# Optimization experiments

Hardware: AMD Instinct MI355X
Metric: run time of the kernel (lower is better)

## Reference

```python
import jax, jax.numpy as jnp
import numpy as np

B, T, NC, WD, UNITS = 128, 256, 128, 512, 512
IN_DIM = NC + WD + NC  # x_char + x_word + one-hot prev word


def setup_inputs() -> dict:
    key = jax.random.key(0)
    ks = jax.random.split(key, 7)
    scale = 0.05  # keep gates out of saturation
    return {
        "x_char": jax.random.normal(ks[0], (B, T, NC), jnp.float32),
        "x_word": jax.random.normal(ks[1], (B, T, WD), jnp.float32),
        "W": jax.random.normal(ks[2], (IN_DIM, 4 * UNITS), jnp.float32) * scale,
        "U": jax.random.normal(ks[3], (UNITS, 4 * UNITS), jnp.float32) * scale,
        "b": jnp.zeros((4 * UNITS,), jnp.float32),
        "Ws": jax.random.normal(ks[4], (UNITS, NC), jnp.float32) * scale,
        "bs": jnp.zeros((NC,), jnp.float32),
    }


def reference(x_char, x_word, W, U, b, Ws, bs):
    Bsz, Tlen, nclasses = x_char.shape
    units = U.shape[0]
    # time-major, concat char+word features (matches x_shuffled in original)
    x_t = jnp.concatenate(
        [jnp.swapaxes(x_char, 0, 1), jnp.swapaxes(x_word, 0, 1)], axis=-1
    )  # [T, B, NC+WD]
    word0 = jnp.full((Bsz, nclasses), 1e-5, x_char.dtype)  # start_char
    h0 = jnp.zeros((Bsz, units), x_char.dtype)
    c0 = jnp.zeros((Bsz, units), x_char.dtype)

    def step(carry, x_i):
        word_vec, h, c = carry
        ins = jnp.concatenate([x_i, word_vec], axis=1)  # [B, IN_DIM]
        z = ins @ W + h @ U + b  # [B, 4*units]; Keras gate order i,f,c,o
        zi, zf, zg, zo = jnp.split(z, 4, axis=1)
        i = jax.nn.sigmoid(zi)
        f = jax.nn.sigmoid(zf)
        g = jnp.tanh(zg)
        o = jax.nn.sigmoid(zo)
        c_new = f * c + i * g
        h_new = o * jnp.tanh(c_new)
        probs = jax.nn.softmax(h_new @ Ws + bs, axis=-1)
        idx = jnp.argmax(probs, axis=1)  # [B]
        word_vec_new = jax.nn.one_hot(idx, nclasses, dtype=x_char.dtype)
        return (word_vec_new, h_new, c_new), idx

    _, idxs = jax.lax.scan(step, (word0, h0, c0), x_t)  # idxs: [T, B]
    return jnp.swapaxes(idxs, 0, 1)  # [B, T] int word indices
```

## Files before the change

### kernel.cpp

```cpp
#include <hip/hip_runtime.h>
#include <math.h>

#define BSZ   128
#define TLEN  256
#define NCLS  128
#define WDIM  512
#define XDIM  640
#define G4    2048

#define BT    16
#define JTS   16
#define NBLK  256
#define NTHR  512
#define KCH   8

#define H_OFF    0
#define LOG_OFF  131072
#define W0_OFF   180224
#define FLAG_OFF 182272

typedef unsigned long long ull;

__device__ __forceinline__ float sigmoidf_(float x) {
  return 1.0f / (1.0f + expf(-x));
}

__device__ __forceinline__ float4 ld_dev16(const float* p) {
  const ull* q = (const ull*)p;
  ull a = __hip_atomic_load(q,     __ATOMIC_RELAXED, __HIP_MEMORY_SCOPE_AGENT);
  ull b = __hip_atomic_load(q + 1, __ATOMIC_RELAXED, __HIP_MEMORY_SCOPE_AGENT);
  float4 r;
  ((ull*)&r)[0] = a;
  ((ull*)&r)[1] = b;
  return r;
}

__global__ void setup_kernel(const float* __restrict__ W,
                             const float* __restrict__ bias,
                             float* __restrict__ ws) {
  int tid = blockIdx.x * blockDim.x + threadIdx.x;
  for (int i = tid; i < 3 * BSZ * NCLS; i += 64 * 256)
    ws[LOG_OFF + i] = 0.0f;
  if (tid < 4096)
    ((unsigned int*)(ws + FLAG_OFF))[tid] = 0u;
  if (tid < G4) {
    float s = 0.0f;
    #pragma unroll 4
    for (int r = 0; r < NCLS; ++r)
      s += W[(size_t)(XDIM + r) * G4 + tid];
    ws[W0_OFF + tid] = bias[tid] + 1e-5f * s;
  }
}

__global__ void __launch_bounds__(NTHR, 1)
lstm_main(const float* __restrict__ xc, const float* __restrict__ xw,
          const float* __restrict__ W,  const float* __restrict__ U,
          const float* __restrict__ bias, const float* __restrict__ Wsm,
          const float* __restrict__ bsv, int* __restrict__ out,
          float* __restrict__ ws)
{
  __shared__ float U_lds[512 * 64];
  __shared__ float ins_lds[2][2176];
  __shared__ float wsm_lds[16 * 128];
  __shared__ float hl_lds[16 * 17];
  __shared__ int   idx_lds[BT];

  float* zred  = &ins_lds[0][0];
  float* Wt    = &ins_lds[0][0];
  float* red_v = zred;
  int*   red_i = (int*)(zred + 528);

  const int tid = threadIdx.x;
  const int blk = blockIdx.x;
  const int grp = blk & 7;
  const int jt  = blk >> 3;
  const int b0  = grp * BT;
  const int j0  = jt * JTS;

  const int gb  = tid & 15;
  const int gg  = (tid >> 4) & 3;
  const int j4  = (tid >> 6) & 3;
  const int kh  = tid >> 8;
  const int c0  = gg * 512 + j0 + j4 * 4;
  const int cc0 = gg * 16 + j4 * 4;

  const int srow = tid >> 5;
  const int sseg = tid & 31;

  const int ub = tid >> 5;
  const int um = tid & 31;

  const int vb = (tid >> 4) & 15;
  const int vj = tid & 15;

  float* hbuf   = ws + H_OFF;
  float* logits = ws + LOG_OFF;
  unsigned int* flags = (unsigned int*)(ws + FLAG_OFF);
  unsigned int* myflag   = flags + (grp * 32 + jt) * 16;
  unsigned int* pollflag = flags + (grp * 32 + (tid & 31)) * 16;

  {
    int cc  = tid & 63;
    int col = (cc >> 4) * 512 + j0 + (cc & 15);
    int k0  = tid >> 6;
    for (int kk = 0; kk < 64; ++kk) {
      int k = kk * 8 + k0;
      U_lds[k * 64 + cc] = U[(size_t)k * G4 + col];
    }
  }
  {
    int row = tid >> 5, col4 = tid & 31;
    *(float4*)(&wsm_lds[row * 128 + col4 * 4]) =
        *(const float4*)(Wsm + (size_t)(j0 + row) * NCLS + col4 * 4);
  }

  float4 xq[KCH];
  auto chunk_gemm = [&](int tt0) {
    #pragma unroll
    for (int s = 0; s < KCH; ++s) xq[s] = make_float4(0.f, 0.f, 0.f, 0.f);
    #pragma unroll 1
    for (int kt = 0; kt < 10; ++kt) {
      int id0 = tid,       k0t = id0 >> 4, cg0 = id0 & 15;
      int id1 = tid + 512, k1t = id1 >> 4, cg1 = id1 & 15;
      int col0 = (cg0 >> 2) * 512 + j0 + (cg0 & 3) * 4;
      int col1 = (cg1 >> 2) * 512 + j0 + (cg1 & 3) * 4;
      float4 wv0 = *(const float4*)(W + (size_t)(kt * 64 + k0t) * G4 + col0);
      float4 wv1 = *(const float4*)(W + (size_t)(kt * 64 + k1t) * G4 + col1);
      __syncthreads();
      *(float4*)(Wt + k0t * 64 + cg0 * 4) = wv0;
      *(float4*)(Wt + k1t * 64 + cg1 * 4) = wv1;
      __syncthreads();
      const float* wp = Wt + (kh * 32) * 64 + cc0;
      #pragma unroll
      for (int s = 0; s < KCH; ++s) {
        int tt = tt0 + s;
        const float* src = (kt < 2)
          ? xc + ((size_t)(b0 + gb) * TLEN + tt) * NCLS + kt * 64 + kh * 32
          : xw + ((size_t)(b0 + gb) * TLEN + tt) * WDIM + (kt * 64 - 128) + kh * 32;
        float xr[32];
        #pragma unroll
        for (int i = 0; i < 8; ++i)
          *(float4*)(&xr[4 * i]) = *(const float4*)(src + 4 * i);
        #pragma unroll
        for (int kk = 0; kk < 32; ++kk) {
          float a = xr[kk];
          float4 w4 = *(const float4*)(wp + kk * 64);
          xq[s].x = fmaf(a, w4.x, xq[s].x);
          xq[s].y = fmaf(a, w4.y, xq[s].y);
          xq[s].z = fmaf(a, w4.z, xq[s].z);
          xq[s].w = fmaf(a, w4.w, xq[s].w);
        }
      }
    }
  };

  float creg = 0.0f;

  __syncthreads();
  chunk_gemm(0);
  __syncthreads();

  for (int t = 0; t < TLEN; ++t) {
    float4 acc = xq[0];
    #pragma unroll
    for (int s = 0; s < KCH - 1; ++s) xq[s] = xq[s + 1];

    if (t == 0) {
      if (kh == 0) {
        const float4 w0 = *(const float4*)(ws + W0_OFF + c0);
        acc.x += w0.x; acc.y += w0.y; acc.z += w0.z; acc.w += w0.w;
      }
    } else {
      {
        const float* lsrc = logits + ((t + 2) % 3) * (BSZ * NCLS)
                          + (b0 + ub) * NCLS + um * 4;
        const float4 bb = *(const float4*)(bsv + um * 4);
        float4 lv = ld_dev16(lsrc);
        float bv = lv.x + bb.x; int bi = um * 4;
        if (lv.y + bb.y > bv) { bv = lv.y + bb.y; bi = um * 4 + 1; }
        if (lv.z + bb.z > bv) { bv = lv.z + bb.z; bi = um * 4 + 2; }
        if (lv.w + bb.w > bv) { bv = lv.w + bb.w; bi = um * 4 + 3; }
        red_v[ub * 33 + um] = bv; red_i[ub * 33 + um] = bi;
        float* lz = logits + ((t + 1) % 3) * (BSZ * NCLS) + b0 * NCLS;
        if (tid < 64)
          __hip_atomic_store(&lz[jt * 64 + tid], 0.0f,
                             __ATOMIC_RELAXED, __HIP_MEMORY_SCOPE_AGENT);
        __syncthreads();
        if (um == 0) {
          float v = red_v[ub * 33]; int vi = red_i[ub * 33];
          #pragma unroll
          for (int s = 1; s < 32; ++s) {
            float v2 = red_v[ub * 33 + s];
            int   i2 = red_i[ub * 33 + s];
            if (v2 > v || (v2 == v && i2 < vi)) { v = v2; vi = i2; }
          }
          idx_lds[ub] = vi;
          if (jt == 0) out[(b0 + ub) * TLEN + (t - 1)] = vi;
        }
        __syncthreads();
      }
      if (kh == 0) {
        int wr = XDIM + idx_lds[gb];
        const float4 b4 = *(const float4*)(bias + c0);
        const float4 w4 = *(const float4*)(W + (size_t)wr * G4 + c0);
        acc.x += b4.x + w4.x;  acc.y += b4.y + w4.y;
        acc.z += b4.z + w4.z;  acc.w += b4.w + w4.w;
      }
      {
        const float* hprev = hbuf + ((t + 1) & 1) * (BSZ * 512);
        {
          float4 r = ld_dev16(hprev + (size_t)(b0 + srow) * 512 + sseg * 4);
          *(float4*)(&ins_lds[0][srow * 132 + sseg * 4]) = r;
          __syncthreads();
        }
        #pragma unroll 1
        for (int ch = 0; ch < 4; ++ch) {
          float4 nxt;
          if (ch + 1 < 4) {
            nxt = ld_dev16(hprev + (size_t)(b0 + srow) * 512
                           + (ch + 1) * 128 + sseg * 4);
          }
          const float* up = U_lds + (ch * 128 + kh * 64) * 64 + cc0;
          const float* ip = &ins_lds[ch & 1][gb * 132 + kh * 64];
          #pragma unroll 8
          for (int kk = 0; kk < 64; ++kk) {
            float a = ip[kk];
            float4 u4 = *(const float4*)(up + kk * 64);
            acc.x = fmaf(a, u4.x, acc.x);
            acc.y = fmaf(a, u4.y, acc.y);
            acc.z = fmaf(a, u4.z, acc.z);
            acc.w = fmaf(a, u4.w, acc.w);
          }
          if (ch + 1 < 4) {
            *(float4*)(&ins_lds[(ch + 1) & 1][srow * 132 + sseg * 4]) = nxt;
            __syncthreads();
          }
        }
      }
    }

    *(float4*)(zred + (gb * 2 + kh) * 68 + cc0) = acc;
    __syncthreads();

    if (tid < 256) {
      float zi = zred[(vb * 2) * 68 +  0 + vj] + zred[(vb * 2 + 1) * 68 +  0 + vj];
      float zf = zred[(vb * 2) * 68 + 16 + vj] + zred[(vb * 2 + 1) * 68 + 16 + vj];
      float zg = zred[(vb * 2) * 68 + 32 + vj] + zred[(vb * 2 + 1) * 68 + 32 + vj];
      float zo = zred[(vb * 2) * 68 + 48 + vj] + zred[(vb * 2 + 1) * 68 + 48 + vj];
      float iv = sigmoidf_(zi);
      float fv = sigmoidf_(zf);
      float gv = tanhf(zg);
      float ov = sigmoidf_(zo);
      creg = fv * creg + iv * gv;
      float hn = ov * tanhf(creg);
      __hip_atomic_store(hbuf + (t & 1) * (BSZ * 512)
                         + (size_t)(b0 + vb) * 512 + j0 + vj, hn,
                         __ATOMIC_RELAXED, __HIP_MEMORY_SCOPE_AGENT);
      hl_lds[vb * 17 + vj] = hn;
    }
    __syncthreads();

    {
      float p0 = 0.f, p1 = 0.f, p2 = 0.f, p3 = 0.f;
      #pragma unroll
      for (int j = 0; j < 16; ++j) {
        float hv = hl_lds[ub * 17 + j];
        const float4 wv = *(const float4*)(&wsm_lds[j * 128 + um * 4]);
        p0 = fmaf(hv, wv.x, p0); p1 = fmaf(hv, wv.y, p1);
        p2 = fmaf(hv, wv.z, p2); p3 = fmaf(hv, wv.w, p3);
      }
      float* ld = logits + (t % 3) * (BSZ * NCLS)
                + (size_t)(b0 + ub) * NCLS + um * 4;
      atomicAdd(ld + 0, p0); atomicAdd(ld + 1, p1);
      atomicAdd(ld + 2, p2); atomicAdd(ld + 3, p3);
    }

    __syncthreads();
    if (tid == 0)
      __hip_atomic_store(myflag, (unsigned)(t + 1),
                         __ATOMIC_RELAXED, __HIP_MEMORY_SCOPE_AGENT);
    if (((t + 1) & (KCH - 1)) == 0 && t + 1 < TLEN)
      chunk_gemm(t + 1);
    if (tid < 64) {
      const unsigned tgt = (unsigned)(t + 1);
      for (;;) {
        unsigned v = __hip_atomic_load(pollflag, __ATOMIC_RELAXED,
                                       __HIP_MEMORY_SCOPE_AGENT);
        if (__all(v >= tgt)) break;
        __builtin_amdgcn_s_sleep(1);
      }
    }
    __syncthreads();
  }

  if (jt == 0) {
    const float* lsrc = logits + ((TLEN - 1) % 3) * (BSZ * NCLS)
                      + (b0 + ub) * NCLS + um * 4;
    const float4 bb = *(const float4*)(bsv + um * 4);
    float4 lv = ld_dev16(lsrc);
    float bv = lv.x + bb.x; int bi = um * 4;
    if (lv.y + bb.y > bv) { bv = lv.y + bb.y; bi = um * 4 + 1; }
    if (lv.z + bb.z > bv) { bv = lv.z + bb.z; bi = um * 4 + 2; }
    if (lv.w + bb.w > bv) { bv = lv.w + bb.w; bi = um * 4 + 3; }
    __syncthreads();
    red_v[ub * 33 + um] = bv; red_i[ub * 33 + um] = bi;
    __syncthreads();
    if (um == 0) {
      float v = red_v[ub * 33]; int vi = red_i[ub * 33];
      #pragma unroll
      for (int s = 1; s < 32; ++s) {
        float v2 = red_v[ub * 33 + s];
        int   i2 = red_i[ub * 33 + s];
        if (v2 > v || (v2 == v && i2 < vi)) { v = v2; vi = i2; }
      }
      out[(b0 + ub) * TLEN + (TLEN - 1)] = vi;
    }
  }
}

extern "C" void kernel_launch(void* const* d_in, const int* in_sizes, int n_in,
                              void* d_out, int out_size, void* d_ws, size_t ws_size,
                              hipStream_t stream) {
  (void)in_sizes; (void)n_in; (void)out_size; (void)ws_size;
  const float* xc  = (const float*)d_in[0];
  const float* xw  = (const float*)d_in[1];
  const float* W   = (const float*)d_in[2];
  const float* U   = (const float*)d_in[3];
  const float* b   = (const float*)d_in[4];
  const float* Wsm = (const float*)d_in[5];
  const float* bs  = (const float*)d_in[6];
  int*   out = (int*)d_out;
  float* ws  = (float*)d_ws;

  hipLaunchKernelGGL(setup_kernel, dim3(64), dim3(256), 0, stream, W, b, ws);

  void* args[] = { (void*)&xc, (void*)&xw, (void*)&W, (void*)&U, (void*)&b,
                   (void*)&Wsm, (void*)&bs, (void*)&out, (void*)&ws };
  hipLaunchCooperativeKernel((const void*)lstm_main, dim3(NBLK), dim3(NTHR),
                             args, 0, stream);
}
```

Baseline: 8.739 ms.

## Register-block recurrent h·U matmul over 4 batch rows in two waves

The recurrent h@U product now runs on only 128 threads (two wavefronts split over k halves), each computing a 4-batch by 4-column register tile with float4 loads of h, instead of 512 threads each doing 1x4 with scalar h loads. The input projection precompute also processes four timesteps per pass to reuse each W load across four x rows. Gate pre-activations are reduced across four partial-sum banks. This cuts LDS traffic per FMA but concentrates the serial per-step matmul on fewer waves, which risks longer latency on the critical recurrent path.

```diff
diff --git a/kernel.cpp b/kernel.cpp
--- a/kernel.cpp
+++ b/kernel.cpp
@@ -20,6 +20,8 @@
 #define FLAG_OFF 182272
 
 typedef unsigned long long ull;
+
+#define ZB(bank, b, c) ins[(bank) * 1120 + (b) * 70 + (c)]
 
 __device__ __forceinline__ float sigmoidf_(float x) {
   return 1.0f / (1.0f + expf(-x));
@@ -60,15 +62,14 @@
           float* __restrict__ ws)
 {
   __shared__ float U_lds[512 * 64];
-  __shared__ float ins_lds[2][2176];
+  __shared__ float ins[4480];
   __shared__ float wsm_lds[16 * 128];
   __shared__ float hl_lds[16 * 17];
   __shared__ int   idx_lds[BT];
 
-  float* zred  = &ins_lds[0][0];
-  float* Wt    = &ins_lds[0][0];
-  float* red_v = zred;
-  int*   red_i = (int*)(zred + 528);
+  float* Wt    = ins;
+  float* red_v = ins;
+  int*   red_i = (int*)(ins + 528);
 
   const int tid = threadIdx.x;
   const int blk = blockIdx.x;
@@ -81,8 +82,13 @@
   const int gg  = (tid >> 4) & 3;
   const int j4  = (tid >> 6) & 3;
   const int kh  = tid >> 8;
-  const int c0  = gg * 512 + j0 + j4 * 4;
   const int cc0 = gg * 16 + j4 * 4;
+
+  const int gkh = tid >> 6;
+  const int bt  = (tid >> 4) & 3;
+  const int ct  = tid & 15;
+  const int mcc = (ct >> 2) * 16 + (ct & 3) * 4;
+  const int gc0 = (ct >> 2) * 512 + j0 + (ct & 3) * 4;
 
   const int srow = tid >> 5;
   const int sseg = tid & 31;
@@ -131,24 +137,39 @@
       *(float4*)(Wt + k1t * 64 + cg1 * 4) = wv1;
       __syncthreads();
       const float* wp = Wt + (kh * 32) * 64 + cc0;
-      #pragma unroll
-      for (int s = 0; s < KCH; ++s) {
-        int tt = tt0 + s;
-        const float* src = (kt < 2)
-          ? xc + ((size_t)(b0 + gb) * TLEN + tt) * NCLS + kt * 64 + kh * 32
-          : xw + ((size_t)(b0 + gb) * TLEN + tt) * WDIM + (kt * 64 - 128) + kh * 32;
-        float xr[32];
-        #pragma unroll
-        for (int i = 0; i < 8; ++i)
-          *(float4*)(&xr[4 * i]) = *(const float4*)(src + 4 * i);
+      #pragma unroll 1
+      for (int sh = 0; sh < 2; ++sh) {
+        float xr0[32], xr1[32], xr2[32], xr3[32];
+        {
+          int tt = tt0 + sh * 4;
+          const float* s0 = (kt < 2)
+            ? xc + ((size_t)(b0 + gb) * TLEN + tt) * NCLS + kt * 64 + kh * 32
+            : xw + ((size_t)(b0 + gb) * TLEN + tt) * WDIM + (kt * 64 - 128) + kh * 32;
+          #pragma unroll
+          for (int i = 0; i < 8; ++i) *(float4*)(&xr0[4*i]) = *(const float4*)(s0 + 4*i);
+          const float* s1 = s0 + ((kt < 2) ? NCLS : WDIM);
+          #pragma unroll
+          for (int i = 0; i < 8; ++i) *(float4*)(&xr1[4*i]) = *(const float4*)(s1 + 4*i);
+          const float* s2 = s1 + ((kt < 2) ? NCLS : WDIM);
+          #pragma unroll
+          for (int i = 0; i < 8; ++i) *(float4*)(&xr2[4*i]) = *(const float4*)(s2 + 4*i);
+          const float* s3 = s2 + ((kt < 2) ? NCLS : WDIM);
+          #pragma unroll
+          for (int i = 0; i < 8; ++i) *(float4*)(&xr3[4*i]) = *(const float4*)(s3 + 4*i);
+        }
         #pragma unroll
         for (int kk = 0; kk < 32; ++kk) {
-          float a = xr[kk];
           float4 w4 = *(const float4*)(wp + kk * 64);
-          xq[s].x = fmaf(a, w4.x, xq[s].x);
-          xq[s].y = fmaf(a, w4.y, xq[s].y);
-          xq[s].z = fmaf(a, w4.z, xq[s].z);
-          xq[s].w = fmaf(a, w4.w, xq[s].w);
+          float a0 = xr0[kk], a1 = xr1[kk], a2 = xr2[kk], a3 = xr3[kk];
+          float4* q = &xq[sh * 4];
+          q[0].x = fmaf(a0, w4.x, q[0].x); q[0].y = fmaf(a0, w4.y, q[0].y);
+          q[0].z = fmaf(a0, w4.z, q[0].z); q[0].w = fmaf(a0, w4.w, q[0].w);
+          q[1].x = fmaf(a1, w4.x, q[1].x); q[1].y = fmaf(a1, w4.y, q[1].y);
+          q[1].z = fmaf(a1, w4.z, q[1].z); q[1].w = fmaf(a1, w4.w, q[1].w);
+          q[2].x = fmaf(a2, w4.x, q[2].x); q[2].y = fmaf(a2, w4.y, q[2].y);
+          q[2].z = fmaf(a2, w4.z, q[2].z); q[2].w = fmaf(a2, w4.w, q[2].w);
+          q[3].x = fmaf(a3, w4.x, q[3].x); q[3].y = fmaf(a3, w4.y, q[3].y);
+          q[3].z = fmaf(a3, w4.z, q[3].z); q[3].w = fmaf(a3, w4.w, q[3].w);
         }
       }
     }
@@ -161,14 +182,18 @@
   __syncthreads();
 
   for (int t = 0; t < TLEN; ++t) {
-    float4 acc = xq[0];
+    float4 xv = xq[0];
     #pragma unroll
     for (int s = 0; s < KCH - 1; ++s) xq[s] = xq[s + 1];
 
+    float4 acc[4];
+    acc[0] = acc[1] = acc[2] = acc[3] = make_float4(0.f, 0.f, 0.f, 0.f);
+    float4 brw[4];
+
     if (t == 0) {
-      if (kh == 0) {
-        const float4 w0 = *(const float4*)(ws + W0_OFF + c0);
-        acc.x += w0.x; acc.y += w0.y; acc.z += w0.z; acc.w += w0.w;
+      if (tid < 128 && gkh == 0) {
+        const float4 w0 = *(const float4*)(ws + W0_OFF + gc0);
+        brw[0] = brw[1] = brw[2] = brw[3] = w0;
       }
     } else {
       {
@@ -199,54 +224,87 @@
         }
         __syncthreads();
       }
-      if (kh == 0) {
-        int wr = XDIM + idx_lds[gb];
-        const float4 b4 = *(const float4*)(bias + c0);
-        const float4 w4 = *(const float4*)(W + (size_t)wr * G4 + c0);
-        acc.x += b4.x + w4.x;  acc.y += b4.y + w4.y;
-        acc.z += b4.z + w4.z;  acc.w += b4.w + w4.w;
+      if (tid < 128 && gkh == 0) {
+        const float4 b4 = *(const float4*)(bias + gc0);
+        #pragma unroll
+        for (int r = 0; r < 4; ++r) {
+          int wr = XDIM + idx_lds[bt * 4 + r];
+          const float4 w4 = *(const float4*)(W + (size_t)wr * G4 + gc0);
+          brw[r] = make_float4(b4.x + w4.x, b4.y + w4.y,
+                               b4.z + w4.z, b4.w + w4.w);
+        }
       }
       {
         const float* hprev = hbuf + ((t + 1) & 1) * (BSZ * 512);
-        {
-          float4 r = ld_dev16(hprev + (size_t)(b0 + srow) * 512 + sseg * 4);
-          *(float4*)(&ins_lds[0][srow * 132 + sseg * 4]) = r;
-          __syncthreads();
-        }
+        float4 hreg = ld_dev16(hprev + (size_t)(b0 + srow) * 512 + sseg * 4);
+        *(float4*)(&ins[srow * 140 + sseg * 4]) = hreg;
+        __syncthreads();
         #pragma unroll 1
         for (int ch = 0; ch < 4; ++ch) {
-          float4 nxt;
-          if (ch + 1 < 4) {
-            nxt = ld_dev16(hprev + (size_t)(b0 + srow) * 512
-                           + (ch + 1) * 128 + sseg * 4);
+          float4 hnext;
+          if (ch + 1 < 4)
+            hnext = ld_dev16(hprev + (size_t)(b0 + srow) * 512
+                             + (ch + 1) * 128 + sseg * 4);
+          if (tid < 128 && gkh == (ch >> 1)) {
+            const float* bp = &ins[(ch & 1) * 2240];
+            const float* up = &U_lds[(ch * 128) * 64 + mcc];
+            #pragma unroll 4
+            for (int kk4 = 0; kk4 < 32; ++kk4) {
+              float4 a0 = *(const float4*)(bp + (bt * 4 + 0) * 140 + kk4 * 4);
+              float4 a1 = *(const float4*)(bp + (bt * 4 + 1) * 140 + kk4 * 4);
+              float4 a2 = *(const float4*)(bp + (bt * 4 + 2) * 140 + kk4 * 4);
+              float4 a3 = *(const float4*)(bp + (bt * 4 + 3) * 140 + kk4 * 4);
+              const float* u = up + kk4 * 256;
+              float4 u0 = *(const float4*)(u);
+              float4 u1 = *(const float4*)(u + 64);
+              float4 u2 = *(const float4*)(u + 128);
+              float4 u3 = *(const float4*)(u + 192);
+              acc[0].x = fmaf(a0.x,u0.x,fmaf(a0.y,u1.x,fmaf(a0.z,u2.x,fmaf(a0.w,u3.x,acc[0].x))));
+              acc[0].y = fmaf(a0.x,u0.y,fmaf(a0.y,u1.y,fmaf(a0.z,u2.y,fmaf(a0.w,u3.y,acc[0].y))));
+              acc[0].z = fmaf(a0.x,u0.z,fmaf(a0.y,u1.z,fmaf(a0.z,u2.z,fmaf(a0.w,u3.z,acc[0].z))));
+              acc[0].w = fmaf(a0.x,u0.w,fmaf(a0.y,u1.w,fmaf(a0.z,u2.w,fmaf(a0.w,u3.w,acc[0].w))));
+              acc[1].x = fmaf(a1.x,u0.x,fmaf(a1.y,u1.x,fmaf(a1.z,u2.x,fmaf(a1.w,u3.x,acc[1].x))));
+              acc[1].y = fmaf(a1.x,u0.y,fmaf(a1.y,u1.y,fmaf(a1.z,u2.y,fmaf(a1.w,u3.y,acc[1].y))));
+              acc[1].z = fmaf(a1.x,u0.z,fmaf(a1.y,u1.z,fmaf(a1.z,u2.z,fmaf(a1.w,u3.z,acc[1].z))));
+              acc[1].w = fmaf(a1.x,u0.w,fmaf(a1.y,u1.w,fmaf(a1.z,u2.w,fmaf(a1.w,u3.w,acc[1].w))));
+              acc[2].x = fmaf(a2.x,u0.x,fmaf(a2.y,u1.x,fmaf(a2.z,u2.x,fmaf(a2.w,u3.x,acc[2].x))));
+              acc[2].y = fmaf(a2.x,u0.y,fmaf(a2.y,u1.y,fmaf(a2.z,u2.y,fmaf(a2.w,u3.y,acc[2].y))));
+              acc[2].z = fmaf(a2.x,u0.z,fmaf(a2.y,u1.z,fmaf(a2.z,u2.z,fmaf(a2.w,u3.z,acc[2].z))));
+              acc[2].w = fmaf(a2.x,u0.w,fmaf(a2.y,u1.w,fmaf(a2.z,u2.w,fmaf(a2.w,u3.w,acc[2].w))));
+              acc[3].x = fmaf(a3.x,u0.x,fmaf(a3.y,u1.x,fmaf(a3.z,u2.x,fmaf(a3.w,u3.x,acc[3].x))));
+              acc[3].y = fmaf(a3.x,u0.y,fmaf(a3.y,u1.y,fmaf(a3.z,u2.y,fmaf(a3.w,u3.y,acc[3].y))));
+              acc[3].z = fmaf(a3.x,u0.z,fmaf(a3.y,u1.z,fmaf(a3.z,u2.z,fmaf(a3.w,u3.z,acc[3].z))));
+              acc[3].w = fmaf(a3.x,u0.w,fmaf(a3.y,u1.w,fmaf(a3.z,u2.w,fmaf(a3.w,u3.w,acc[3].w))));
+            }
           }
-          const float* up = U_lds + (ch * 128 + kh * 64) * 64 + cc0;
-          const float* ip = &ins_lds[ch & 1][gb * 132 + kh * 64];
-          #pragma unroll 8
-          for (int kk = 0; kk < 64; ++kk) {
-            float a = ip[kk];
-            float4 u4 = *(const float4*)(up + kk * 64);
-            acc.x = fmaf(a, u4.x, acc.x);
-            acc.y = fmaf(a, u4.y, acc.y);
-            acc.z = fmaf(a, u4.z, acc.z);
-            acc.w = fmaf(a, u4.w, acc.w);
-          }
-          if (ch + 1 < 4) {
-            *(float4*)(&ins_lds[(ch + 1) & 1][srow * 132 + sseg * 4]) = nxt;
-            __syncthreads();
-          }
-        }
-      }
-    }
-
-    *(float4*)(zred + (gb * 2 + kh) * 68 + cc0) = acc;
+          if (ch + 1 < 4)
+            *(float4*)(&ins[((ch + 1) & 1) * 2240 + srow * 140 + sseg * 4]) = hnext;
+          __syncthreads();
+        }
+      }
+    }
+
+    if (t == 0) __syncthreads();
+    *(float4*)(&ZB(kh, gb, cc0)) = xv;
+    if (tid < 128) {
+      if (gkh == 0) {
+        #pragma unroll
+        for (int r = 0; r < 4; ++r) {
+          acc[r].x += brw[r].x; acc[r].y += brw[r].y;
+          acc[r].z += brw[r].z; acc[r].w += brw[r].w;
+        }
+      }
+      #pragma unroll
+      for (int r = 0; r < 4; ++r)
+        *(float4*)(&ZB(2 + gkh, bt * 4 + r, mcc)) = acc[r];
+    }
     __syncthreads();
 
     if (tid < 256) {
-      float zi = zred[(vb * 2) * 68 +  0 + vj] + zred[(vb * 2 + 1) * 68 +  0 + vj];
-      float zf = zred[(vb * 2) * 68 + 16 + vj] + zred[(vb * 2 + 1) * 68 + 16 + vj];
-      float zg = zred[(vb * 2) * 68 + 32 + vj] + zred[(vb * 2 + 1) * 68 + 32 + vj];
-      float zo = zred[(vb * 2) * 68 + 48 + vj] + zred[(vb * 2 + 1) * 68 + 48 + vj];
+      float zi = ZB(0,vb, 0+vj) + ZB(1,vb, 0+vj) + ZB(2,vb, 0+vj) + ZB(3,vb, 0+vj);
+      float zf = ZB(0,vb,16+vj) + ZB(1,vb,16+vj) + ZB(2,vb,16+vj) + ZB(3,vb,16+vj);
+      float zg = ZB(0,vb,32+vj) + ZB(1,vb,32+vj) + ZB(2,vb,32+vj) + ZB(3,vb,32+vj);
+      float zo = ZB(0,vb,48+vj) + ZB(1,vb,48+vj) + ZB(2,vb,48+vj) + ZB(3,vb,48+vj);
       float iv = sigmoidf_(zi);
       float fv = sigmoidf_(zf);
       float gv = tanhf(zg);
```

Result: slower. 14.49 ms (+65.8%).
